# Performance work log

Hardware: AMD Instinct MI355X
Metric: run time of the kernel (lower is better)

The kernel has to match this reference:

```python
import jax, jax.numpy as jnp
import numpy as np

N = 4096        # nbCou_nodes
F = 30          # factorDimCou (input feature dim of CFactor)
H = 30          # hid_units[0] (GAT hidden dim)
E = 32          # emb_dim
R = 4           # relations: ICCI, ICCSI, CTC, CCC
NEG_INF = -1e9


def setup_inputs() -> dict:
    key = jax.random.key(0)
    ks = jax.random.split(key, 12)
    seq = jax.random.normal(ks[0], (1, N, F), dtype=jnp.float32)
    u = jax.random.uniform(ks[1], (R, N, N), dtype=jnp.float32)
    bias_mats = jnp.where(u < 0.05, 0.0, NEG_INF).astype(jnp.float32)
    s = 0.1
    W = jax.random.normal(ks[2], (R, F, H), dtype=jnp.float32) * s          # conv_no_bias kernels
    a1 = jax.random.normal(ks[3], (R, H, 1), dtype=jnp.float32) * s        # conv_f1 kernels
    b1 = jax.random.normal(ks[4], (R, 1), dtype=jnp.float32) * s           # conv_f1 bias
    a2 = jax.random.normal(ks[5], (R, H, 1), dtype=jnp.float32) * s        # conv_f2 kernels
    b2 = jax.random.normal(ks[6], (R, 1), dtype=jnp.float32) * s           # conv_f2 bias
    bias_zero = jnp.zeros((R, H), dtype=jnp.float32)                        # attn_head bias_zero
    Wd = jax.random.normal(ks[7], (R, H, E), dtype=jnp.float32) * s        # HIN_MLP* kernels
    bd = jax.random.normal(ks[8], (R, E), dtype=jnp.float32) * s           # HIN_MLP* biases
    return {"seq": seq, "bias_mats": bias_mats, "W": W, "a1": a1, "b1": b1,
            "a2": a2, "b2": b2, "bias_zero": bias_zero, "Wd": Wd, "bd": bd}


def _gat_head(x, biasr, Wr, a1r, b1r, a2r, b2r, bzr):
    # x: [N, F]; biasr: [N, N]; one attn_head with identity activation + residual (F == H)
    fts = x @ Wr                                   # Conv1D(H, 1, no bias) -> [N, H]
    f1 = fts @ a1r + b1r                           # [N, 1]
    f2 = fts @ a2r + b2r                           # [N, 1]
    logits = f1 + f2.T                             # [N, N]
    coefs = jax.nn.softmax(jax.nn.leaky_relu(logits, 0.2) + biasr, axis=-1)
    vals = coefs @ fts                             # [N, H]
    return vals + bzr + x                          # bias_zero + residual (identity activation)


def reference(seq, bias_mats, W, a1, b1, a2, b2, bias_zero, Wd, bd):
    x = seq[0]                                     # [N, F]
    # one head per relation (n_heads[-1] == 1), vmapped over the 4 relation graphs
    outs = jax.vmap(_gat_head, in_axes=(None, 0, 0, 0, 0, 0, 0, 0))(
        x, bias_mats, W, a1, b1, a2, b2, bias_zero)        # [R, N, H]
    # Factor_comp = (HIN_MLPICCI(.) + HIN_MLPICCSI(.) + HIN_MLPCTC(.) + HIN_MLPCCC(.)) / 4
    comb = jnp.einsum('rnh,rhe->rne', outs, Wd) + bd[:, None, :]
    return (comb.sum(axis=0) / 4.0)[None]          # [1, N, E]
```

## Files before the change

### kernel.cpp

```cpp
#include <hip/hip_runtime.h>
#include <hip/hip_bf16.h>

#define N_NODES 4096
#define FDIM 30
#define HDIM 30
#define EDIM 32
#define NREL 4
#define FTS_LD 32
#define CAPH 192

__global__ __launch_bounds__(256) void prep_kernel(
    const float* __restrict__ x, const float* __restrict__ W,
    const float* __restrict__ a1, const float* __restrict__ b1,
    const float* __restrict__ a2, const float* __restrict__ b2,
    float* __restrict__ fts, float* __restrict__ f1, float* __restrict__ f2)
{
    int pair = blockIdx.x * 8 + (threadIdx.x >> 5);
    int lane = threadIdx.x & 31;
    int r = pair >> 12;
    int n = pair & (N_NODES - 1);

    const float* xr = x + n * FDIM;
    const float* Wr = W + r * FDIM * HDIM + lane;

    float acc = 0.f;
    if (lane < HDIM) {
#pragma unroll
        for (int f = 0; f < FDIM; ++f)
            acc = fmaf(xr[f], Wr[f * HDIM], acc);
    }
    fts[(size_t)pair * FTS_LD + lane] = acc;

    float s1 = (lane < HDIM) ? acc * a1[r * HDIM + lane] : 0.f;
    float s2 = (lane < HDIM) ? acc * a2[r * HDIM + lane] : 0.f;
#pragma unroll
    for (int o = 16; o >= 1; o >>= 1) {
        s1 += __shfl_xor(s1, o, 32);
        s2 += __shfl_xor(s2, o, 32);
    }
    if (lane == 0) {
        f1[pair] = s1 + b1[r];
        f2[pair] = s2 + b2[r];
    }
}

__global__ __launch_bounds__(512, 8) void gat_kernel(
    const float* __restrict__ bias, const float* __restrict__ x,
    const float* __restrict__ fts, const float* __restrict__ f1,
    const float* __restrict__ f2, const float* __restrict__ bz,
    const float* __restrict__ Wd, const float* __restrict__ bd,
    float* __restrict__ out)
{
    __shared__ float wlist[NREL][2 * CAPH];
    __shared__ unsigned short jlist[NREL][2 * CAPH];
    __shared__ float pv[8][32];
    __shared__ float ps[8];
    __shared__ float y_sh[NREL][32];

    const int i = blockIdx.x;
    const int t = threadIdx.x;
    const int wid = t >> 6;
    const int lane = t & 63;
    const int r = wid >> 1;
    const int half = wid & 1;

    const float4* brow = (const float4*)(bias + ((size_t)(r * N_NODES + i)) * N_NODES)
                         + half * 512;
    float* wl = wlist[r] + half * CAPH;
    unsigned short* jl = jlist[r] + half * CAPH;

    int cnt = 0;

#pragma unroll 4
    for (int it = 0; it < 8; ++it) {
        float4 b4 = brow[it * 64 + lane];
        int jb = (half * 512 + it * 64 + lane) * 4;
#define DO_ELEM(K, BK)                                                        \
        {                                                                     \
            bool pred = (BK >= 0.f);                                          \
            unsigned long long m = __ballot(pred);                            \
            if (pred) {                                                       \
                int pos = cnt + (int)__builtin_amdgcn_mbcnt_hi(               \
                    (unsigned)(m >> 32),                                      \
                    __builtin_amdgcn_mbcnt_lo((unsigned)m, 0u));              \
                if (pos < CAPH) jl[pos] = (unsigned short)(jb + K);           \
            }                                                                 \
            cnt += (int)__popcll(m);                                          \
        }
        DO_ELEM(0, b4.x)
        DO_ELEM(1, b4.y)
        DO_ELEM(2, b4.z)
        DO_ELEM(3, b4.w)
#undef DO_ELEM
    }
    const int M = cnt < CAPH ? cnt : CAPH;

    const float f1i = f1[r * N_NODES + i];
    const float* f2r = f2 + r * N_NODES;
    float sw = 0.f;
    for (int p = lane; p < M; p += 64) {
        int j = (int)jl[p];
        float l = f1i + f2r[j];
        l = fmaxf(l, 0.2f * l);
        float w = __expf(l);
        wl[p] = w;
        sw += w;
    }
#pragma unroll
    for (int o = 32; o >= 1; o >>= 1) sw += __shfl_xor(sw, o);

    const int h = lane & 31;
    const int c = lane >> 5;
    const float* fb = fts + (size_t)r * N_NODES * FTS_LD + h;
    float acc = 0.f;
#pragma unroll 8
    for (int p = c; p < M; p += 2)
        acc = fmaf(wl[p], fb[(int)jl[p] * FTS_LD], acc);
    acc += __shfl_xor(acc, 32);

    if (lane < 32) pv[wid][lane] = acc;
    if (lane == 0) ps[wid] = sw;
    __syncthreads();

    if (t < 128) {
        int g = t >> 5, h2 = t & 31;
        float v = pv[2 * g][h2] + pv[2 * g + 1][h2];
        float s = ps[2 * g] + ps[2 * g + 1];
        if (s == 0.f) s = 1.f;
        float extra = (h2 < HDIM) ? bz[g * HDIM + h2] + x[i * FDIM + h2] : 0.f;
        y_sh[g][h2] = v / s + extra;
    }
    __syncthreads();

    if (t < EDIM) {
        float e = 0.f;
#pragma unroll
        for (int r2 = 0; r2 < NREL; ++r2) {
            e += bd[r2 * EDIM + t];
            const float* Wdr = Wd + r2 * HDIM * EDIM + t;
#pragma unroll
            for (int h2 = 0; h2 < HDIM; ++h2)
                e = fmaf(y_sh[r2][h2], Wdr[h2 * EDIM], e);
        }
        out[(size_t)i * EDIM + t] = e * 0.25f;
    }
}

extern "C" void kernel_launch(void* const* d_in, const int* in_sizes, int n_in,
                              void* d_out, int out_size, void* d_ws, size_t ws_size,
                              hipStream_t stream)
{
    const float* seq  = (const float*)d_in[0];
    const float* bias = (const float*)d_in[1];
    const float* W    = (const float*)d_in[2];
    const float* a1   = (const float*)d_in[3];
    const float* b1   = (const float*)d_in[4];
    const float* a2   = (const float*)d_in[5];
    const float* b2   = (const float*)d_in[6];
    const float* bz   = (const float*)d_in[7];
    const float* Wd   = (const float*)d_in[8];
    const float* bd   = (const float*)d_in[9];
    float* out = (float*)d_out;

    float* fts = (float*)d_ws;
    float* f1  = fts + (size_t)NREL * N_NODES * FTS_LD;
    float* f2  = f1 + NREL * N_NODES;

    prep_kernel<<<NREL * N_NODES / 8, 256, 0, stream>>>(
        seq, W, a1, b1, a2, b2, fts, f1, f2);
    gat_kernel<<<N_NODES, 512, 0, stream>>>(
        bias, seq, fts, f1, f2, bz, Wd, bd, out);
}
```

Measured before the change: 88.46 us.

## Split mask compaction into separate streaming kernel writing global index lists

Moves the scan of the dense bias mask into its own lightweight kernel that writes compacted neighbour index lists and counts to workspace. The GAT kernel then reads these lists instead of scanning the 256MB mask itself. The intent is to let the bandwidth-bound mask scan run at higher occupancy, separate from the gather/accumulate work. The cost is an extra launch plus a global round-trip for the index lists, about 12MB written and then read back.

```diff
diff --git a/kernel.cpp b/kernel.cpp
--- a/kernel.cpp
+++ b/kernel.cpp
@@ -44,15 +44,52 @@
     }
 }
 
+__global__ __launch_bounds__(256, 8) void stream_kernel(
+    const float* __restrict__ bias, unsigned short* __restrict__ jlg,
+    int* __restrict__ cnts)
+{
+    const int wave = blockIdx.x * 4 + (threadIdx.x >> 6);
+    const int lane = threadIdx.x & 63;
+    const int row  = wave >> 1;
+    const int half = wave & 1;
+
+    const float4* p = (const float4*)(bias + (size_t)row * N_NODES) + half * 512;
+    unsigned short* jseg = jlg + (size_t)(row * 2 + half) * CAPH;
+
+    int cnt = 0;
+#pragma unroll
+    for (int it = 0; it < 8; ++it) {
+        float4 b4 = p[it * 64 + lane];
+        int jb = (half * 512 + it * 64 + lane) * 4;
+#define DO_ELEM(K, BK)                                                        \
+        {                                                                     \
+            bool pred = (BK >= 0.f);                                          \
+            unsigned long long m = __ballot(pred);                            \
+            if (pred) {                                                       \
+                int pos = cnt + (int)__builtin_amdgcn_mbcnt_hi(               \
+                    (unsigned)(m >> 32),                                      \
+                    __builtin_amdgcn_mbcnt_lo((unsigned)m, 0u));              \
+                if (pos < CAPH) jseg[pos] = (unsigned short)(jb + K);         \
+            }                                                                 \
+            cnt += (int)__popcll(m);                                          \
+        }
+        DO_ELEM(0, b4.x)
+        DO_ELEM(1, b4.y)
+        DO_ELEM(2, b4.z)
+        DO_ELEM(3, b4.w)
+#undef DO_ELEM
+    }
+    if (lane == 0) cnts[row * 2 + half] = cnt < CAPH ? cnt : CAPH;
+}
+
 __global__ __launch_bounds__(512, 8) void gat_kernel(
-    const float* __restrict__ bias, const float* __restrict__ x,
-    const float* __restrict__ fts, const float* __restrict__ f1,
-    const float* __restrict__ f2, const float* __restrict__ bz,
-    const float* __restrict__ Wd, const float* __restrict__ bd,
-    float* __restrict__ out)
+    const float* __restrict__ x, const float* __restrict__ fts,
+    const float* __restrict__ f1, const float* __restrict__ f2,
+    const unsigned short* __restrict__ jlg, const int* __restrict__ cnts,
+    const float* __restrict__ bz, const float* __restrict__ Wd,
+    const float* __restrict__ bd, float* __restrict__ out)
 {
     __shared__ float wlist[NREL][2 * CAPH];
-    __shared__ unsigned short jlist[NREL][2 * CAPH];
     __shared__ float pv[8][32];
     __shared__ float ps[8];
     __shared__ float y_sh[NREL][32];
@@ -64,36 +101,10 @@
     const int r = wid >> 1;
     const int half = wid & 1;
 
-    const float4* brow = (const float4*)(bias + ((size_t)(r * N_NODES + i)) * N_NODES)
-                         + half * 512;
+    const int seg = (r * N_NODES + i) * 2 + half;
+    const int M = cnts[seg];
+    const unsigned short* jl = jlg + (size_t)seg * CAPH;
     float* wl = wlist[r] + half * CAPH;
-    unsigned short* jl = jlist[r] + half * CAPH;
-
-    int cnt = 0;
-
-#pragma unroll 4
-    for (int it = 0; it < 8; ++it) {
-        float4 b4 = brow[it * 64 + lane];
-        int jb = (half * 512 + it * 64 + lane) * 4;
-#define DO_ELEM(K, BK)                                                        \
-        {                                                                     \
-            bool pred = (BK >= 0.f);                                          \
-            unsigned long long m = __ballot(pred);                            \
-            if (pred) {                                                       \
-                int pos = cnt + (int)__builtin_amdgcn_mbcnt_hi(               \
-                    (unsigned)(m >> 32),                                      \
-                    __builtin_amdgcn_mbcnt_lo((unsigned)m, 0u));              \
-                if (pos < CAPH) jl[pos] = (unsigned short)(jb + K);           \
-            }                                                                 \
-            cnt += (int)__popcll(m);                                          \
-        }
-        DO_ELEM(0, b4.x)
-        DO_ELEM(1, b4.y)
-        DO_ELEM(2, b4.z)
-        DO_ELEM(3, b4.w)
-#undef DO_ELEM
-    }
-    const int M = cnt < CAPH ? cnt : CAPH;
 
     const float f1i = f1[r * N_NODES + i];
     const float* f2r = f2 + r * N_NODES;
@@ -108,6 +119,7 @@
     }
 #pragma unroll
     for (int o = 32; o >= 1; o >>= 1) sw += __shfl_xor(sw, o);
+    __builtin_amdgcn_wave_barrier();
 
     const int h = lane & 31;
     const int c = lane >> 5;
@@ -165,9 +177,12 @@
     float* fts = (float*)d_ws;
     float* f1  = fts + (size_t)NREL * N_NODES * FTS_LD;
     float* f2  = f1 + NREL * N_NODES;
+    unsigned short* jlg = (unsigned short*)(f2 + NREL * N_NODES);
+    int* cnts = (int*)(jlg + (size_t)NREL * N_NODES * 2 * CAPH);
 
     prep_kernel<<<NREL * N_NODES / 8, 256, 0, stream>>>(
         seq, W, a1, b1, a2, b2, fts, f1, f2);
+    stream_kernel<<<NREL * N_NODES * 2 / 4, 256, 0, stream>>>(bias, jlg, cnts);
     gat_kernel<<<N_NODES, 512, 0, stream>>>(
-        bias, seq, fts, f1, f2, bz, Wd, bd, out);
+        seq, fts, f1, f2, jlg, cnts, bz, Wd, bd, out);
 }
```

Result: slower. 104.8 us (+18.5%).

## Process eight rows of one relation per block and combine relations in separate kernel

Applied to the files above, without the earlier changes.

Each block now handles 8 consecutive rows of a single relation, with each wave owning one row for the softmax and aggregation stages. The wave-level compaction appends edge indices into shared per-row lists through LDS atomics, and the per-wave stages synchronise only at wave level. Per-relation outputs go to a workspace and a third kernel averages the four relations. The bias stream is read in larger contiguous chunks and per-row work is balanced across waves, at the cost of an extra launch, extra global traffic for the workspace, and atomic contention on the row counters.

```diff
diff --git a/kernel.cpp b/kernel.cpp
--- a/kernel.cpp
+++ b/kernel.cpp
@@ -7,7 +7,8 @@
 #define EDIM 32
 #define NREL 4
 #define FTS_LD 32
-#define CAPH 192
+#define CAP 384
+#define GRP 8
 
 __global__ __launch_bounds__(256) void prep_kernel(
     const float* __restrict__ x, const float* __restrict__ W,
@@ -44,48 +45,50 @@
     }
 }
 
-__global__ __launch_bounds__(512, 8) void gat_kernel(
+__global__ __launch_bounds__(512, 8) void gat8_kernel(
     const float* __restrict__ bias, const float* __restrict__ x,
     const float* __restrict__ fts, const float* __restrict__ f1,
     const float* __restrict__ f2, const float* __restrict__ bz,
     const float* __restrict__ Wd, const float* __restrict__ bd,
-    float* __restrict__ out)
+    float* __restrict__ zws)
 {
-    __shared__ float wlist[NREL][2 * CAPH];
-    __shared__ unsigned short jlist[NREL][2 * CAPH];
-    __shared__ float pv[8][32];
-    __shared__ float ps[8];
-    __shared__ float y_sh[NREL][32];
+    __shared__ unsigned short jl[GRP][CAP];
+    __shared__ float wl[GRP][CAP];
+    __shared__ float y_sh[GRP][32];
+    __shared__ int cnt[GRP];
 
-    const int i = blockIdx.x;
     const int t = threadIdx.x;
     const int wid = t >> 6;
     const int lane = t & 63;
-    const int r = wid >> 1;
-    const int half = wid & 1;
+    const int r = blockIdx.x >> 9;
+    const int g = blockIdx.x & 511;
+    const int row0 = g * GRP;
 
-    const float4* brow = (const float4*)(bias + ((size_t)(r * N_NODES + i)) * N_NODES)
-                         + half * 512;
-    float* wl = wlist[r] + half * CAPH;
-    unsigned short* jl = jlist[r] + half * CAPH;
+    if (t < GRP) cnt[t] = 0;
+    __syncthreads();
 
-    int cnt = 0;
+    const unsigned long long below = (1ull << lane) - 1ull;
+    const float4* gp = (const float4*)(bias + ((size_t)r * N_NODES + row0) * N_NODES);
 
 #pragma unroll 4
-    for (int it = 0; it < 8; ++it) {
-        float4 b4 = brow[it * 64 + lane];
-        int jb = (half * 512 + it * 64 + lane) * 4;
+    for (int it = 0; it < 16; ++it) {
+        const int chunk = it * 8 + wid;
+        float4 b4 = gp[chunk * 64 + lane];
+        const int row8 = chunk >> 4;
+        const int jb = ((chunk & 15) * 64 + lane) * 4;
 #define DO_ELEM(K, BK)                                                        \
         {                                                                     \
             bool pred = (BK >= 0.f);                                          \
             unsigned long long m = __ballot(pred);                            \
-            if (pred) {                                                       \
-                int pos = cnt + (int)__builtin_amdgcn_mbcnt_hi(               \
-                    (unsigned)(m >> 32),                                      \
-                    __builtin_amdgcn_mbcnt_lo((unsigned)m, 0u));              \
-                if (pos < CAPH) jl[pos] = (unsigned short)(jb + K);           \
+            if (m) {                                                          \
+                int base;                                                     \
+                if (lane == 0) base = atomicAdd(&cnt[row8], (int)__popcll(m));\
+                base = __shfl(base, 0);                                       \
+                if (pred) {                                                   \
+                    int pos = base + (int)__popcll(m & below);                \
+                    if (pos < CAP) jl[row8][pos] = (unsigned short)(jb + K);  \
+                }                                                             \
             }                                                                 \
-            cnt += (int)__popcll(m);                                          \
         }
         DO_ELEM(0, b4.x)
         DO_ELEM(1, b4.y)
@@ -93,21 +96,25 @@
         DO_ELEM(3, b4.w)
 #undef DO_ELEM
     }
-    const int M = cnt < CAPH ? cnt : CAPH;
+    __syncthreads();
 
-    const float f1i = f1[r * N_NODES + i];
+    const int node = row0 + wid;
+    const int M = cnt[wid] < CAP ? cnt[wid] : CAP;
+    const float f1i = f1[r * N_NODES + node];
     const float* f2r = f2 + r * N_NODES;
     float sw = 0.f;
     for (int p = lane; p < M; p += 64) {
-        int j = (int)jl[p];
+        int j = (int)jl[wid][p];
         float l = f1i + f2r[j];
         l = fmaxf(l, 0.2f * l);
         float w = __expf(l);
-        wl[p] = w;
+        wl[wid][p] = w;
         sw += w;
     }
 #pragma unroll
     for (int o = 32; o >= 1; o >>= 1) sw += __shfl_xor(sw, o);
+    if (sw == 0.f) sw = 1.f;
+    __builtin_amdgcn_wave_barrier();
 
     const int h = lane & 31;
     const int c = lane >> 5;
@@ -115,35 +122,31 @@
     float acc = 0.f;
 #pragma unroll 8
     for (int p = c; p < M; p += 2)
-        acc = fmaf(wl[p], fb[(int)jl[p] * FTS_LD], acc);
+        acc = fmaf(wl[wid][p], fb[(int)jl[wid][p] * FTS_LD], acc);
     acc += __shfl_xor(acc, 32);
 
-    if (lane < 32) pv[wid][lane] = acc;
-    if (lane == 0) ps[wid] = sw;
-    __syncthreads();
+    if (lane < 32)
+        y_sh[wid][lane] = (lane < HDIM)
+            ? acc / sw + bz[r * HDIM + lane] + x[node * FDIM + lane] : 0.f;
+    __builtin_amdgcn_wave_barrier();
 
-    if (t < 128) {
-        int g = t >> 5, h2 = t & 31;
-        float v = pv[2 * g][h2] + pv[2 * g + 1][h2];
-        float s = ps[2 * g] + ps[2 * g + 1];
-        if (s == 0.f) s = 1.f;
-        float extra = (h2 < HDIM) ? bz[g * HDIM + h2] + x[i * FDIM + h2] : 0.f;
-        y_sh[g][h2] = v / s + extra;
+    if (lane < EDIM) {
+        float e = bd[r * EDIM + lane];
+        const float* Wdr = Wd + r * HDIM * EDIM + lane;
+#pragma unroll 10
+        for (int h2 = 0; h2 < HDIM; ++h2)
+            e = fmaf(y_sh[wid][h2], Wdr[h2 * EDIM], e);
+        zws[((size_t)r * N_NODES + node) * EDIM + lane] = e;
     }
-    __syncthreads();
+}
 
-    if (t < EDIM) {
-        float e = 0.f;
-#pragma unroll
-        for (int r2 = 0; r2 < NREL; ++r2) {
-            e += bd[r2 * EDIM + t];
-            const float* Wdr = Wd + r2 * HDIM * EDIM + t;
-#pragma unroll
-            for (int h2 = 0; h2 < HDIM; ++h2)
-                e = fmaf(y_sh[r2][h2], Wdr[h2 * EDIM], e);
-        }
-        out[(size_t)i * EDIM + t] = e * 0.25f;
-    }
+__global__ __launch_bounds__(256) void combine_kernel(
+    const float* __restrict__ zws, float* __restrict__ out)
+{
+    const int idx = blockIdx.x * 256 + threadIdx.x;
+    const int NE = N_NODES * EDIM;
+    float s = zws[idx] + zws[idx + NE] + zws[idx + 2 * NE] + zws[idx + 3 * NE];
+    out[idx] = s * 0.25f;
 }
 
 extern "C" void kernel_launch(void* const* d_in, const int* in_sizes, int n_in,
@@ -165,9 +168,11 @@
     float* fts = (float*)d_ws;
     float* f1  = fts + (size_t)NREL * N_NODES * FTS_LD;
     float* f2  = f1 + NREL * N_NODES;
+    float* zws = f2 + NREL * N_NODES;
 
     prep_kernel<<<NREL * N_NODES / 8, 256, 0, stream>>>(
         seq, W, a1, b1, a2, b2, fts, f1, f2);
-    gat_kernel<<<N_NODES, 512, 0, stream>>>(
-        bias, seq, fts, f1, f2, bz, Wd, bd, out);
+    gat8_kernel<<<NREL * N_NODES / GRP, 512, 0, stream>>>(
+        bias, seq, fts, f1, f2, bz, Wd, bd, zws);
+    combine_kernel<<<N_NODES * EDIM / 256, 256, 0, stream>>>(zws, out);
 }
```

After: 76.76 us. 13.2% less time.
